# Kernel optimization log

Hardware: AMD Instinct MI355X
Metric: run time of the kernel (lower is better)

The kernel has to match this reference:

```python
import jax, jax.numpy as jnp
import numpy as np

IN, H, OUT = 8, 256, 24  # input_size, hidden_size, output_size
B, T = 2048, 256


def _gate_step(hx, x, Wx, Wh, b):
    # Fused version of the 8 per-gate Linears: one [.,IN]@[IN,4H] + one [.,H]@[H,4H]
    gates = x @ Wx + hx @ Wh + b            # [B, 4H]
    i, f, o, g = jnp.split(gates, 4, axis=-1)
    i, f, o = jax.nn.sigmoid(i), jax.nn.sigmoid(f), jax.nn.sigmoid(o)
    g = jnp.tanh(g)
    # NOTE: in the original code cx is never reassigned, so it stays zeros and
    # cy = cx*f + i*g == i*g on every step. We replicate that exactly.
    cy = i * g
    return o * jnp.tanh(cy)


def setup_inputs() -> dict:
    key = jax.random.key(0)
    ks = jax.random.split(key, 9)
    s = 0.05
    return {
        "inputs0": jax.random.normal(ks[0], (B, T, IN), jnp.float32),
        "inputs1": jax.random.normal(ks[1], (B, OUT - 1), jnp.float32),
        # concatenated gate weights, order [i | f | o | c]
        "Wx": jax.random.normal(ks[2], (IN, 4 * H), jnp.float32) * s,
        "Wh": jax.random.normal(ks[3], (H, 4 * H), jnp.float32) * s,
        "b": jax.random.normal(ks[4], (4 * H,), jnp.float32) * s,  # bx + bh folded
        "Wy": jax.random.normal(ks[5], (H, 1), jnp.float32) * s,
        "by": jax.random.normal(ks[6], (1,), jnp.float32) * s,
        # fresh random Linear(1, IN) per decoder step in the original -> per-step params
        "dec_w": jax.random.normal(ks[7], (OUT - 1, IN), jnp.float32) * s,
        "dec_b": jax.random.normal(ks[8], (OUT - 1, IN), jnp.float32) * s,
    }


def reference(inputs0, inputs1, Wx, Wh, b, Wy, by, dec_w, dec_b):
    bsz = inputs0.shape[0]
    h0 = jnp.zeros((bsz, H), inputs0.dtype)

    # ---- encoder: scan over time (strict recurrence) ----
    x_seq = jnp.transpose(inputs0, (1, 0, 2))  # [T, B, IN]

    def enc_step(h, x):
        return _gate_step(h, x, Wx, Wh, b), None

    h, _ = jax.lax.scan(enc_step, h0, x_seq)
    hy0 = h @ Wy + by                           # [B, 1]

    # ---- decoder: OUT-1 steps, each with its own fresh 1->IN linear ----
    x1_seq = jnp.transpose(inputs1, (1, 0))[: OUT - 1]  # [OUT-1, B]

    def dec_step(h, inp):
        x1, w, bb = inp
        x = x1[:, None] * w[None, :] + bb[None, :]      # [B, IN]
        h = _gate_step(h, x, Wx, Wh, b)
        return h, h @ Wy + by                            # y: [B, 1]

    _, ys = jax.lax.scan(dec_step, h, (x1_seq, dec_w, dec_b))  # ys: [OUT-1, B, 1]

    hy = jnp.concatenate([hy0, jnp.transpose(ys[..., 0], (1, 0))], axis=1)  # [B, OUT]
    return hy
```

## Files before the change

### kernel.cpp

```cpp
#include <hip/hip_runtime.h>


typedef short bf16x8 __attribute__((ext_vector_type(8)));
typedef float f32x4 __attribute__((ext_vector_type(4)));

#define T_ENC 256
#define N_DEC 23
#define NSTEP 279
#define HSTR 296
#define AG_T 36
#define LDS_T 18

__device__ __forceinline__ short f2bf(float f) {
  unsigned u = __float_as_uint(f);
  u = (u + 0x7fffu + ((u >> 16) & 1u)) >> 16;
  return (short)u;
}
__device__ __forceinline__ float bf2f(short s) {
  return __uint_as_float(((unsigned)(unsigned short)s) << 16);
}

#if __has_builtin(__builtin_amdgcn_rcpf)
#define RCPF(x) __builtin_amdgcn_rcpf(x)
#else
#define RCPF(x) (1.0f / (x))
#endif

__device__ __forceinline__ float sigm(float x) { return RCPF(1.0f + __expf(-x)); }
__device__ __forceinline__ float tanhf_fast(float x) {
  return 1.0f - 2.0f * RCPF(__expf(2.0f * x) + 1.0f);
}

__global__ void pack_kernel(const float* __restrict__ Wx, const float* __restrict__ Wh,
                            const float* __restrict__ b, short* __restrict__ Wpack) {
  int tau = blockIdx.x;
  int l = threadIdx.x;
  int n_tile = tau / 9, kt = tau % 9;
  int w = n_tile / 6, t = n_tile % 6;
  int gate = t >> 1, loc = t & 1;
  int base = (gate == 0) ? 0 : (gate == 1 ? 512 : 768);
  int c = l & 15, q = l >> 4;
  int oc = base + w * 32 + loc * 16 + c;
  bf16x8 v;
#pragma unroll
  for (int e = 0; e < 8; ++e) {
    int k = kt * 32 + q * 8 + e;
    float f;
    if (k < 256)       f = Wh[k * 1024 + oc];
    else if (k < 264)  f = Wx[(k - 256) * 1024 + oc];
    else if (k == 264) f = b[oc];
    else               f = 0.0f;
    v[e] = f2bf(f);
  }
  ((bf16x8*)Wpack)[tau * 64 + l] = v;
}

__global__ __launch_bounds__(512, 2) void lstm_kernel(
    const float* __restrict__ inputs0, const float* __restrict__ inputs1,
    const float* __restrict__ Wy, const float* __restrict__ by,
    const float* __restrict__ dec_w, const float* __restrict__ dec_b,
    const short* __restrict__ Wpack, float* __restrict__ out) {
  __shared__ __align__(16) short B_lds[8 * LDS_T * 512];
  __shared__ __align__(16) short hbuf[8 * HSTR];
  __shared__ float Wy_lds[256];
  __shared__ float ypart[128];

  const int tid = threadIdx.x;
  const int wg = blockIdx.x;
  const int lane = tid & 63;
  const int w = tid >> 6;
  const int q = lane >> 4;
  const int c = lane & 15;

  const bf16x8* wp = (const bf16x8*)Wpack;

  bf16x8 Bag[AG_T];
#pragma unroll
  for (int r = 0; r < AG_T; ++r) {
    bf16x8 t0 = wp[(w * 54 + r) * 64 + lane];
    asm("" : "=a"(Bag[r]) : "0"(t0));
  }
#pragma unroll
  for (int j = 0; j < LDS_T; ++j) {
    bf16x8 v = wp[(w * 54 + AG_T + j) * 64 + lane];
    *(bf16x8*)(B_lds + (w * LDS_T + j) * 512 + lane * 8) = v;
  }

  for (int i = tid; i < 8 * HSTR; i += 512) hbuf[i] = 0;
  if (tid < 256) Wy_lds[tid] = Wy[tid];
  __syncthreads();

  if (tid < 64) {
    int m = tid >> 3, kk = tid & 7;
    hbuf[m * HSTR + 256 + kk] = f2bf(inputs0[((wg * 8 + m) * 256 + 0) * 8 + kk]);
  }
  if (tid < 8) hbuf[tid * HSTR + 264] = (short)0x3F80;
  const float byv = by[0];
  __syncthreads();

#define RDA(kt) (*(const bf16x8*)(hbuf + (c & 7) * HSTR + (kt) * 32 + q * 8))
#define LDSB(j) (*(const bf16x8*)(B_lds + (w * LDS_T + (j)) * 512 + lane * 8))

  for (int s = 0; s < NSTEP; ++s) {
    float xv = 0.0f;
    const bool do_x = (tid < 64) && (s + 1 < NSTEP);
    const int xm = tid >> 3, xk = tid & 7;
    if (do_x) {
      int sn = s + 1;
      if (sn < T_ENC) {
        xv = inputs0[((wg * 8 + xm) * 256 + sn) * 8 + xk];
      } else {
        int d = sn - T_ENC;
        xv = inputs1[(wg * 8 + xm) * N_DEC + d] * dec_w[d * 8 + xk] + dec_b[d * 8 + xk];
      }
    }

    bf16x8 A3[3];
    A3[0] = RDA(0); A3[1] = RDA(1); A3[2] = RDA(2);
    f32x4 acc[6];
#pragma unroll
    for (int t = 0; t < 6; ++t) { acc[t][0] = 0.f; acc[t][1] = 0.f; acc[t][2] = 0.f; acc[t][3] = 0.f; }
#pragma unroll
    for (int kt = 0; kt < 9; ++kt) {
      const bf16x8 a = A3[kt % 3];
      acc[0] = __builtin_amdgcn_mfma_f32_16x16x32_bf16(a, Bag[0 * 9 + kt], acc[0], 0, 0, 0);
      acc[1] = __builtin_amdgcn_mfma_f32_16x16x32_bf16(a, Bag[1 * 9 + kt], acc[1], 0, 0, 0);
      acc[2] = __builtin_amdgcn_mfma_f32_16x16x32_bf16(a, Bag[2 * 9 + kt], acc[2], 0, 0, 0);
      acc[3] = __builtin_amdgcn_mfma_f32_16x16x32_bf16(a, Bag[3 * 9 + kt], acc[3], 0, 0, 0);
      acc[4] = __builtin_amdgcn_mfma_f32_16x16x32_bf16(a, LDSB(kt), acc[4], 0, 0, 0);
      acc[5] = __builtin_amdgcn_mfma_f32_16x16x32_bf16(a, LDSB(9 + kt), acc[5], 0, 0, 0);
      if (kt + 3 < 9) A3[kt % 3] = RDA(kt + 3);
    }
    __syncthreads();

    const int qh = q >> 1;
    const f32x4 vi = qh ? acc[1] : acc[0];
    const f32x4 vo = qh ? acc[3] : acc[2];
    const f32x4 vg = qh ? acc[5] : acc[4];
    const int row0 = (q & 1) * 4;
    const int colw = w * 32 + qh * 16 + c;
#pragma unroll
    for (int j = 0; j < 4; ++j) {
      float ii = sigm(vi[j]);
      float oo = sigm(vo[j]);
      float gg = tanhf_fast(vg[j]);
      float h = oo * tanhf_fast(ii * gg);
      hbuf[(row0 + j) * HSTR + colw] = f2bf(h);
    }
    if (do_x) hbuf[xm * HSTR + 256 + xk] = f2bf(xv);
    __syncthreads();

    if (s >= T_ENC - 1) {
      if (tid < 128) {
        int m = tid & 7, kq = tid >> 3;
        const short* hp = hbuf + m * HSTR + kq * 16;
        bf16x8 h0 = *(const bf16x8*)(hp);
        bf16x8 h1 = *(const bf16x8*)(hp + 8);
        float part = 0.0f;
#pragma unroll
        for (int j = 0; j < 8; ++j) {
          part += bf2f(h0[j]) * Wy_lds[kq * 16 + j];
          part += bf2f(h1[j]) * Wy_lds[kq * 16 + 8 + j];
        }
        ypart[tid] = part;
      }
      __syncthreads();
      if (tid < 8) {
        float y = byv;
#pragma unroll
        for (int kq = 0; kq < 16; ++kq) y += ypart[kq * 8 + tid];
        out[(wg * 8 + tid) * 24 + (s - (T_ENC - 1))] = y;
      }
    }
  }
}

extern "C" void kernel_launch(void* const* d_in, const int* in_sizes, int n_in,
                              void* d_out, int out_size, void* d_ws, size_t ws_size,
                              hipStream_t stream) {
  const float* inputs0 = (const float*)d_in[0];
  const float* inputs1 = (const float*)d_in[1];
  const float* Wx      = (const float*)d_in[2];
  const float* Wh      = (const float*)d_in[3];
  const float* b       = (const float*)d_in[4];
  const float* Wy      = (const float*)d_in[5];
  const float* by      = (const float*)d_in[6];
  const float* dec_w   = (const float*)d_in[7];
  const float* dec_b   = (const float*)d_in[8];

  short* Wpack = (short*)d_ws;

  pack_kernel<<<dim3(432), dim3(64), 0, stream>>>(Wx, Wh, b, Wpack);
  lstm_kernel<<<dim3(256), dim3(512), 0, stream>>>(
      inputs0, inputs1, Wy, by, dec_w, dec_b, Wpack, (float*)d_out);
}
```

Baseline: 447.0 us.

## Double-buffer hidden state and split gate MFMAs to overlap activations

```diff
diff --git a/kernel.cpp b/kernel.cpp
--- a/kernel.cpp
+++ b/kernel.cpp
@@ -61,7 +61,7 @@
     const float* __restrict__ dec_w, const float* __restrict__ dec_b,
     const short* __restrict__ Wpack, float* __restrict__ out) {
   __shared__ __align__(16) short B_lds[8 * LDS_T * 512];
-  __shared__ __align__(16) short hbuf[8 * HSTR];
+  __shared__ __align__(16) short hbuf[2][8 * HSTR];
   __shared__ float Wy_lds[256];
   __shared__ float ypart[128];
 
@@ -86,22 +86,29 @@
     *(bf16x8*)(B_lds + (w * LDS_T + j) * 512 + lane * 8) = v;
   }
 
-  for (int i = tid; i < 8 * HSTR; i += 512) hbuf[i] = 0;
+  for (int i = tid; i < 2 * 8 * HSTR; i += 512) hbuf[0][i] = 0;
   if (tid < 256) Wy_lds[tid] = Wy[tid];
   __syncthreads();
 
   if (tid < 64) {
     int m = tid >> 3, kk = tid & 7;
-    hbuf[m * HSTR + 256 + kk] = f2bf(inputs0[((wg * 8 + m) * 256 + 0) * 8 + kk]);
-  }
-  if (tid < 8) hbuf[tid * HSTR + 264] = (short)0x3F80;
+    hbuf[0][m * HSTR + 256 + kk] = f2bf(inputs0[((wg * 8 + m) * 256 + 0) * 8 + kk]);
+  }
+  if (tid < 16)
+    hbuf[tid >> 3][(tid & 7) * HSTR + 264] = (short)0x3F80;
   const float byv = by[0];
   __syncthreads();
 
-#define RDA(kt) (*(const bf16x8*)(hbuf + (c & 7) * HSTR + (kt) * 32 + q * 8))
 #define LDSB(j) (*(const bf16x8*)(B_lds + (w * LDS_T + (j)) * 512 + lane * 8))
 
+  const int qh = q >> 1;
+  const int row0 = (q & 1) * 4;
+  const int colw = w * 32 + qh * 16 + c;
+
   for (int s = 0; s < NSTEP; ++s) {
+    const short* hc = &hbuf[s & 1][0];
+    short* hn = &hbuf[(s + 1) & 1][0];
+
     float xv = 0.0f;
     const bool do_x = (tid < 64) && (s + 1 < NSTEP);
     const int xm = tid >> 3, xk = tid & 7;
@@ -115,45 +122,67 @@
       }
     }
 
-    bf16x8 A3[3];
-    A3[0] = RDA(0); A3[1] = RDA(1); A3[2] = RDA(2);
-    f32x4 acc[6];
-#pragma unroll
-    for (int t = 0; t < 6; ++t) { acc[t][0] = 0.f; acc[t][1] = 0.f; acc[t][2] = 0.f; acc[t][3] = 0.f; }
+    bf16x8 A[9];
+#pragma unroll
+    for (int kt = 0; kt < 9; ++kt)
+      A[kt] = *(const bf16x8*)(hc + (c & 7) * HSTR + kt * 32 + q * 8);
+
+    f32x4 a0, a1;
+    a0[0]=0.f;a0[1]=0.f;a0[2]=0.f;a0[3]=0.f; a1=a0;
 #pragma unroll
     for (int kt = 0; kt < 9; ++kt) {
-      const bf16x8 a = A3[kt % 3];
-      acc[0] = __builtin_amdgcn_mfma_f32_16x16x32_bf16(a, Bag[0 * 9 + kt], acc[0], 0, 0, 0);
-      acc[1] = __builtin_amdgcn_mfma_f32_16x16x32_bf16(a, Bag[1 * 9 + kt], acc[1], 0, 0, 0);
-      acc[2] = __builtin_amdgcn_mfma_f32_16x16x32_bf16(a, Bag[2 * 9 + kt], acc[2], 0, 0, 0);
-      acc[3] = __builtin_amdgcn_mfma_f32_16x16x32_bf16(a, Bag[3 * 9 + kt], acc[3], 0, 0, 0);
-      acc[4] = __builtin_amdgcn_mfma_f32_16x16x32_bf16(a, LDSB(kt), acc[4], 0, 0, 0);
-      acc[5] = __builtin_amdgcn_mfma_f32_16x16x32_bf16(a, LDSB(9 + kt), acc[5], 0, 0, 0);
-      if (kt + 3 < 9) A3[kt % 3] = RDA(kt + 3);
-    }
-    __syncthreads();
-
-    const int qh = q >> 1;
-    const f32x4 vi = qh ? acc[1] : acc[0];
-    const f32x4 vo = qh ? acc[3] : acc[2];
-    const f32x4 vg = qh ? acc[5] : acc[4];
-    const int row0 = (q & 1) * 4;
-    const int colw = w * 32 + qh * 16 + c;
-#pragma unroll
-    for (int j = 0; j < 4; ++j) {
-      float ii = sigm(vi[j]);
-      float oo = sigm(vo[j]);
-      float gg = tanhf_fast(vg[j]);
-      float h = oo * tanhf_fast(ii * gg);
-      hbuf[(row0 + j) * HSTR + colw] = f2bf(h);
-    }
-    if (do_x) hbuf[xm * HSTR + 256 + xk] = f2bf(xv);
+      a0 = __builtin_amdgcn_mfma_f32_16x16x32_bf16(A[kt], Bag[0 * 9 + kt], a0, 0, 0, 0);
+      a1 = __builtin_amdgcn_mfma_f32_16x16x32_bf16(A[kt], Bag[1 * 9 + kt], a1, 0, 0, 0);
+    }
+    float ii[4];
+    {
+      const f32x4 vi = qh ? a1 : a0;
+#pragma unroll
+      for (int j = 0; j < 4; ++j) ii[j] = sigm(vi[j]);
+    }
+    a0[0]=0.f;a0[1]=0.f;a0[2]=0.f;a0[3]=0.f; a1=a0;
+#pragma unroll
+    for (int kt = 0; kt < 9; ++kt) {
+      a0 = __builtin_amdgcn_mfma_f32_16x16x32_bf16(A[kt], Bag[2 * 9 + kt], a0, 0, 0, 0);
+      a1 = __builtin_amdgcn_mfma_f32_16x16x32_bf16(A[kt], Bag[3 * 9 + kt], a1, 0, 0, 0);
+    }
+    float oo[4];
+    {
+      const f32x4 vo = qh ? a1 : a0;
+#pragma unroll
+      for (int j = 0; j < 4; ++j) oo[j] = sigm(vo[j]);
+    }
+    a0[0]=0.f;a0[1]=0.f;a0[2]=0.f;a0[3]=0.f; a1=a0;
+#pragma unroll
+    for (int kt = 0; kt < 9; ++kt) {
+      a0 = __builtin_amdgcn_mfma_f32_16x16x32_bf16(A[kt], LDSB(kt), a0, 0, 0, 0);
+      a1 = __builtin_amdgcn_mfma_f32_16x16x32_bf16(A[kt], LDSB(9 + kt), a1, 0, 0, 0);
+    }
+    float hh[4];
+    {
+      const f32x4 vg = qh ? a1 : a0;
+#pragma unroll
+      for (int j = 0; j < 4; ++j) {
+        float gg = tanhf_fast(vg[j]);
+        hh[j] = oo[j] * tanhf_fast(ii[j] * gg);
+      }
+    }
+    {
+      unsigned pk01, pk23;
+      asm("v_cvt_pk_bf16_f32 %0, %1, %2" : "=v"(pk01) : "v"(hh[0]), "v"(hh[1]));
+      asm("v_cvt_pk_bf16_f32 %0, %1, %2" : "=v"(pk23) : "v"(hh[2]), "v"(hh[3]));
+      hn[(row0 + 0) * HSTR + colw] = (short)(pk01 & 0xffffu);
+      hn[(row0 + 1) * HSTR + colw] = (short)(pk01 >> 16);
+      hn[(row0 + 2) * HSTR + colw] = (short)(pk23 & 0xffffu);
+      hn[(row0 + 3) * HSTR + colw] = (short)(pk23 >> 16);
+    }
+    if (do_x) hn[xm * HSTR + 256 + xk] = f2bf(xv);
     __syncthreads();
 
     if (s >= T_ENC - 1) {
       if (tid < 128) {
         int m = tid & 7, kq = tid >> 3;
-        const short* hp = hbuf + m * HSTR + kq * 16;
+        const short* hp = hn + m * HSTR + kq * 16;
         bf16x8 h0 = *(const bf16x8*)(hp);
         bf16x8 h1 = *(const bf16x8*)(hp + 8);
         float part = 0.0f;
@@ -171,6 +200,7 @@
         for (int kq = 0; kq < 16; ++kq) y += ypart[kq * 8 + tid];
         out[(wg * 8 + tid) * 24 + (s - (T_ENC - 1))] = y;
       }
+      __syncthreads();
     }
   }
 }
```

Measured after the change: 427.0 us. 1.05x faster.
